# Kernel optimization log

Hardware: AMD Instinct MI355X
Metric: run time of the kernel (lower is better)

The kernel has to match this reference:

```python
import jax, jax.numpy as jnp
import numpy as np

N = 50000      # nodes
NE = 800000    # edges (avg degree 16)
DIN = 128      # in_dim / dim_edge
DOUT = 128     # out_dim (total)
H = 8          # heads
DH = DOUT // H # head dim = 16


def setup_inputs() -> dict:
    key = jax.random.key(0)
    ks = jax.random.split(key, 12)
    w = lambda k, shape: (jax.random.normal(k, shape, jnp.float32) / np.sqrt(shape[-1]))
    return {
        "x": jax.random.normal(ks[0], (N, DIN), jnp.float32),
        "edge_attr": jax.random.normal(ks[1], (NE, DIN), jnp.float32),
        "edge_index": jax.random.randint(ks[2], (2, NE), 0, N, dtype=jnp.int32),
        "batch_vec": jnp.zeros((N,), jnp.int32),  # single graph; only used for num_node
        "Wq": w(ks[3], (DOUT, DIN)), "bq": jnp.zeros((DOUT,), jnp.float32),
        "Wk": w(ks[4], (DOUT, DIN)), "bk": jnp.zeros((DOUT,), jnp.float32),
        "We": w(ks[5], (DOUT, DIN)), "be": jnp.zeros((DOUT,), jnp.float32),
        "Wv": w(ks[6], (DOUT, DIN)), "bv": jnp.zeros((DOUT,), jnp.float32),
    }


def reference(x, edge_attr, edge_index, batch_vec, Wq, bq, Wk, bk, We, be, Wv, bv):
    num_node = batch_vec.shape[0]
    # Node projections -> [N, H, DH]
    Qh = (x @ Wq.T + bq).reshape(-1, H, DH)
    Kh = (x @ Wk.T + bk).reshape(-1, H, DH)
    Vh = (x @ Wv.T + bv).reshape(-1, H, DH)
    # Edge projection -> [NE, H, DH]
    E = (edge_attr @ We.T + be).reshape(-1, H, DH)

    src = edge_index[0]
    dst = edge_index[1]
    # edge score: exp(clamp(sum(K_src * Q_dst / sqrt(DH) * E, -1), -5, 5))  [NE, H, 1]
    scale = 1.0 / np.sqrt(DH).astype(np.float32)
    s = jnp.sum((Kh[src] * Qh[dst]) * scale * E, axis=-1)
    score = jnp.exp(jnp.clip(s, -5.0, 5.0))[..., None]

    msg = Vh[src] * score                                   # [NE, H, DH]
    wV = jax.ops.segment_sum(msg, dst, num_segments=num_node)  # [N, H, DH]
    return wV.reshape(num_node, H * DH)
```

## Files before the change

### kernel.cpp

```cpp
#include <hip/hip_runtime.h>
#include <hip/hip_bf16.h>
#include <hip/hip_fp16.h>
#include <cstdint>


typedef float    f32x4  __attribute__((ext_vector_type(4)));
typedef short    bf16x8 __attribute__((ext_vector_type(8)));
typedef int      i32x4  __attribute__((ext_vector_type(4)));
typedef _Float16 f16x8  __attribute__((ext_vector_type(8)));
typedef _Float16 f16x4  __attribute__((ext_vector_type(4)));

#define AP 136
#define EP 132

__device__ __forceinline__ short f2bf(float f) {
    union { float f; uint32_t u; } v; v.f = f;
    uint32_t r = v.u + 0x7FFFu + ((v.u >> 16) & 1u);
    return (short)(r >> 16);
}
__device__ __forceinline__ float bf2f(short s) {
    union { uint32_t u; float f; } v; v.u = ((uint32_t)(uint16_t)s) << 16;
    return v.f;
}
__device__ __forceinline__ int cvt2(float a, float b) {
    float2 t; t.x = a; t.y = b;
    __hip_bfloat162 h = __float22bfloat162_rn(t);
    int r; __builtin_memcpy(&r, &h, 4);
    return r;
}
__device__ __forceinline__ float4 ntload4(const float* p) {
    i32x4 r = __builtin_nontemporal_load((const i32x4*)p);
    float4 f; __builtin_memcpy(&f, &r, 16);
    return f;
}

__global__ __launch_bounds__(256) void convert_weights(
        const float* __restrict__ Wq, const float* __restrict__ bq,
        const float* __restrict__ Wk, const float* __restrict__ bk,
        const float* __restrict__ We, const float* __restrict__ be,
        const float* __restrict__ Wv, const float* __restrict__ bv,
        const int* __restrict__ dstp, int NE,
        short* __restrict__ Whi, short* __restrict__ Wlo, float* __restrict__ ball,
        int* __restrict__ counts) {
    int idx = blockIdx.x * 256 + threadIdx.x;
    int wrow = idx >> 7;
    int k = idx & 127;
    int which = wrow >> 7;
    int r = wrow & 127;
    const float* Wsrc = which == 0 ? Wq : which == 1 ? Wk : which == 2 ? Wv : We;
    float f = Wsrc[r * 128 + k];
    short hi = f2bf(f);
    short lo = f2bf(f - bf2f(hi));
    Whi[idx] = hi; Wlo[idx] = lo;
    if (idx < 512) {
        int wh = idx >> 7; int rr = idx & 127;
        const float* bsrc = wh == 0 ? bq : wh == 1 ? bk : wh == 2 ? bv : be;
        ball[idx] = bsrc[rr];
    }
    for (int i = idx; i < NE; i += 65536)
        atomicAdd(&counts[dstp[i]], 1);
}

__global__ __launch_bounds__(1024) void scan1_kernel(const int* __restrict__ counts,
                                                     int* __restrict__ incl,
                                                     int* __restrict__ partials, int n) {
    __shared__ int sh[1024];
    int t = threadIdx.x;
    int i = blockIdx.x * 1024 + t;
    sh[t] = (i < n) ? counts[i] : 0;
    for (int off = 1; off < 1024; off <<= 1) {
        __syncthreads();
        int xv = (t >= off) ? sh[t - off] : 0;
        __syncthreads();
        sh[t] += xv;
    }
    __syncthreads();
    if (i < n) incl[i] = sh[t];
    if (t == 1023) partials[blockIdx.x] = sh[1023];
}

__global__ __launch_bounds__(1024) void scanB_kernel(const int* __restrict__ counts,
                                                     int* __restrict__ offsets,
                                                     int* __restrict__ cursors,
                                                     const int* __restrict__ partials,
                                                     int n, int total) {
    int pbase = 0;
    for (int b = 0; b < (int)blockIdx.x; ++b) pbase += partials[b];
    int i = blockIdx.x * 1024 + threadIdx.x;
    if (i < n) {
        int off = offsets[i] - counts[i] + pbase;
        offsets[i] = off;
        cursors[i] = off;
    } else if (i == n) {
        offsets[n] = total;
    }
}

__global__ __launch_bounds__(256, 4) void qkv_kernel(
        const float* __restrict__ x,
        const short* __restrict__ Whi, const short* __restrict__ Wlo,
        const float* __restrict__ ball,
        _Float16* __restrict__ Qb, _Float16* __restrict__ Kb, _Float16* __restrict__ Vb,
        int N) {
    __shared__ char lds[64 * AP * 2];
    const int t = threadIdx.x;
    const int m0 = blockIdx.x * 64;

#pragma unroll
    for (int i = 0; i < 4; ++i) {
        int g = t + i * 256;
        int row = g >> 4, c8 = g & 15;
        int grow = m0 + row;
        float4 f0 = {0.f,0.f,0.f,0.f}, f1 = {0.f,0.f,0.f,0.f};
        if (grow < N) {
            const float* p = x + (size_t)grow * 128 + c8 * 8;
            f0 = ntload4(p); f1 = ntload4(p + 4);
        }
        int4 v;
        v.x = cvt2(f0.x, f0.y); v.y = cvt2(f0.z, f0.w);
        v.z = cvt2(f1.x, f1.y); v.w = cvt2(f1.z, f1.w);
        *(int4*)(lds + row * (AP * 2) + c8 * 16) = v;
    }
    __syncthreads();

    const int w = t >> 6, lane = t & 63;
    const int r16 = lane & 15, g16 = lane >> 4;
    const int cb = w * 32;

    for (int ct = 0; ct < 3; ++ct) {
        const int colbase = ct * 128;
        f32x4 acc[4][2];
#pragma unroll
        for (int m = 0; m < 4; ++m)
#pragma unroll
            for (int n = 0; n < 2; ++n) acc[m][n] = (f32x4){0.f,0.f,0.f,0.f};

#pragma unroll
        for (int ks = 0; ks < 4; ++ks) {
            bf16x8 a[4];
#pragma unroll
            for (int m = 0; m < 4; ++m)
                a[m] = *(const bf16x8*)(lds + (m * 16 + r16) * (AP * 2) + ks * 64 + g16 * 16);
            bf16x8 bh2[2], bl2[2];
#pragma unroll
            for (int n = 0; n < 2; ++n) {
                int colg = colbase + cb + n * 16 + r16;
                bh2[n] = *(const bf16x8*)(Whi + colg * 128 + ks * 32 + g16 * 8);
                bl2[n] = *(const bf16x8*)(Wlo + colg * 128 + ks * 32 + g16 * 8);
            }
#pragma unroll
            for (int m = 0; m < 4; ++m)
#pragma unroll
                for (int n = 0; n < 2; ++n) {
                    acc[m][n] = __builtin_amdgcn_mfma_f32_16x16x32_bf16(a[m], bh2[n], acc[m][n], 0, 0, 0);
                    acc[m][n] = __builtin_amdgcn_mfma_f32_16x16x32_bf16(a[m], bl2[n], acc[m][n], 0, 0, 0);
                }
        }
        float bias[2];
#pragma unroll
        for (int n = 0; n < 2; ++n) bias[n] = ball[colbase + cb + n * 16 + r16];

        _Float16* outb = ct == 0 ? Qb : ct == 1 ? Kb : Vb;
#pragma unroll
        for (int m = 0; m < 4; ++m) {
            int grow = m0 + m * 16 + g16 * 4;
#pragma unroll
            for (int r = 0; r < 4; ++r) {
                if (grow + r < N) {
#pragma unroll
                    for (int n = 0; n < 2; ++n)
                        outb[(size_t)(grow + r) * 128 + cb + n * 16 + r16] =
                            (_Float16)(acc[m][n][r] + bias[n]);
                }
            }
        }
    }
}

__global__ __launch_bounds__(256) void edge_kernel(
        const float* __restrict__ ea,
        const int* __restrict__ srcp, const int* __restrict__ dstp,
        const short* __restrict__ Whi, const short* __restrict__ Wlo,
        const float* __restrict__ ball,
        const _Float16* __restrict__ Qb, const _Float16* __restrict__ Kb,
        float* __restrict__ scores, int* __restrict__ cursors,
        int2* __restrict__ ebuf, int NE) {
    __shared__ char lds[64 * EP * 4];
    const int t = threadIdx.x;
    const int e0 = blockIdx.x * 64;

    int sArr[2], dArr[2];
#pragma unroll
    for (int it = 0; it < 2; ++it) {
        int task = t + it * 256;
        int el = task >> 3, h = task & 7;
        int eg = e0 + el;
        bool ok = eg < NE;
        int s = ok ? srcp[eg] : 0;
        int d = ok ? dstp[eg] : 0;
        sArr[it] = s; dArr[it] = d;
        if (ok && h == 0) {
            int pos = atomicAdd(&cursors[d], 1);
            int2 v; v.x = s * 128; v.y = eg * 8;
            ebuf[pos] = v;
        }
    }

#pragma unroll
    for (int i = 0; i < 4; ++i) {
        int g = t + i * 256;
        int row = g >> 4, c8 = g & 15;
        int grow = e0 + row;
        float4 f0 = {0.f,0.f,0.f,0.f}, f1 = {0.f,0.f,0.f,0.f};
        if (grow < NE) {
            const float* p = ea + (size_t)grow * 128 + c8 * 8;
            f0 = ntload4(p); f1 = ntload4(p + 4);
        }
        int4 v;
        v.x = cvt2(f0.x, f0.y); v.y = cvt2(f0.z, f0.w);
        v.z = cvt2(f1.x, f1.y); v.w = cvt2(f1.z, f1.w);
        *(int4*)(lds + row * (AP * 2) + c8 * 16) = v;
    }
    __syncthreads();

    const int w = t >> 6, lane = t & 63;
    const int r16 = lane & 15, g16 = lane >> 4;
    const int cb = w * 32;

    f32x4 acc[4][2];
#pragma unroll
    for (int m = 0; m < 4; ++m)
#pragma unroll
        for (int n = 0; n < 2; ++n) acc[m][n] = (f32x4){0.f,0.f,0.f,0.f};

#pragma unroll
    for (int ks = 0; ks < 4; ++ks) {
        bf16x8 a[4];
#pragma unroll
        for (int m = 0; m < 4; ++m)
            a[m] = *(const bf16x8*)(lds + (m * 16 + r16) * (AP * 2) + ks * 64 + g16 * 16);
        bf16x8 bh2[2], bl2[2];
#pragma unroll
        for (int n = 0; n < 2; ++n) {
            int colg = 384 + cb + n * 16 + r16;
            bh2[n] = *(const bf16x8*)(Whi + colg * 128 + ks * 32 + g16 * 8);
            bl2[n] = *(const bf16x8*)(Wlo + colg * 128 + ks * 32 + g16 * 8);
        }
#pragma unroll
        for (int m = 0; m < 4; ++m)
#pragma unroll
            for (int n = 0; n < 2; ++n) {
                acc[m][n] = __builtin_amdgcn_mfma_f32_16x16x32_bf16(a[m], bh2[n], acc[m][n], 0, 0, 0);
                acc[m][n] = __builtin_amdgcn_mfma_f32_16x16x32_bf16(a[m], bl2[n], acc[m][n], 0, 0, 0);
            }
    }
    float bias[2];
#pragma unroll
    for (int n = 0; n < 2; ++n) bias[n] = ball[384 + cb + n * 16 + r16];

    __syncthreads();
    float* e_lds = (float*)lds;
#pragma unroll
    for (int m = 0; m < 4; ++m)
#pragma unroll
        for (int n = 0; n < 2; ++n)
#pragma unroll
            for (int r = 0; r < 4; ++r) {
                int row = m * 16 + g16 * 4 + r;
                int col = cb + n * 16 + r16;
                e_lds[row * EP + col] = acc[m][n][r] + bias[n];
            }
    __syncthreads();

#pragma unroll
    for (int it = 0; it < 2; ++it) {
        int task = t + it * 256;
        int el = task >> 3, h = task & 7;
        int eg = e0 + el;
        if (eg < NE) {
            const f16x8* Kp = (const f16x8*)(Kb + (size_t)sArr[it] * 128 + h * 16);
            const f16x8* Qp = (const f16x8*)(Qb + (size_t)dArr[it] * 128 + h * 16);
            f16x8 k0 = Kp[0], k1 = Kp[1];
            f16x8 q0 = Qp[0], q1 = Qp[1];
            float dot = 0.f;
#pragma unroll
            for (int j = 0; j < 2; ++j) {
                f32x4 ev0 = *(const f32x4*)(e_lds + el * EP + h * 16 + j * 8);
                f32x4 ev1 = *(const f32x4*)(e_lds + el * EP + h * 16 + j * 8 + 4);
                const f16x8& kk = j == 0 ? k0 : k1;
                const f16x8& qq = j == 0 ? q0 : q1;
#pragma unroll
                for (int r = 0; r < 4; ++r) {
                    dot += ev0[r] * (float)kk[r] * (float)qq[r];
                    dot += ev1[r] * (float)kk[r + 4] * (float)qq[r + 4];
                }
            }
            float sv = fminf(fmaxf(dot * 0.25f, -5.0f), 5.0f);
            scores[(size_t)eg * 8 + h] = __expf(sv);
        }
    }
}

__global__ __launch_bounds__(256) void gather_kernel(
        const int* __restrict__ offsets, const int2* __restrict__ eb,
        const float* __restrict__ scores, const _Float16* __restrict__ Vb,
        float* __restrict__ out, int N) {
    int node = blockIdx.x * 8 + (threadIdx.x >> 5);
    int c4 = threadIdx.x & 31;
    if (node >= N) return;
    int h = c4 >> 2;
    int beg = offsets[node], end = offsets[node + 1];
    f32x4 a0 = {0.f,0.f,0.f,0.f}, a1 = a0, a2 = a0, a3 = a0;
    int j = beg;
    auto vload = [&](int off) -> f32x4 {
        f16x4 v = *(const f16x4*)(Vb + off + c4 * 4);
        return (f32x4){(float)v[0], (float)v[1], (float)v[2], (float)v[3]};
    };
    for (; j + 8 <= end; j += 8) {
        int2 e0 = eb[j],     e1 = eb[j + 1], e2 = eb[j + 2], e3 = eb[j + 3];
        int2 e4 = eb[j + 4], e5 = eb[j + 5], e6 = eb[j + 6], e7 = eb[j + 7];
        f32x4 v0 = vload(e0.x), v1 = vload(e1.x), v2 = vload(e2.x), v3 = vload(e3.x);
        f32x4 v4 = vload(e4.x), v5 = vload(e5.x), v6 = vload(e6.x), v7 = vload(e7.x);
        a0 += scores[e0.y + h] * v0;
        a1 += scores[e1.y + h] * v1;
        a2 += scores[e2.y + h] * v2;
        a3 += scores[e3.y + h] * v3;
        a0 += scores[e4.y + h] * v4;
        a1 += scores[e5.y + h] * v5;
        a2 += scores[e6.y + h] * v6;
        a3 += scores[e7.y + h] * v7;
    }
    for (; j + 4 <= end; j += 4) {
        int2 e0 = eb[j], e1 = eb[j + 1], e2 = eb[j + 2], e3 = eb[j + 3];
        f32x4 v0 = vload(e0.x), v1 = vload(e1.x), v2 = vload(e2.x), v3 = vload(e3.x);
        a0 += scores[e0.y + h] * v0;
        a1 += scores[e1.y + h] * v1;
        a2 += scores[e2.y + h] * v2;
        a3 += scores[e3.y + h] * v3;
    }
    for (; j < end; ++j) {
        int2 e = eb[j];
        a0 += scores[e.y + h] * vload(e.x);
    }
    f32x4 sum = (a0 + a1) + (a2 + a3);
    *(f32x4*)(out + (size_t)node * 128 + c4 * 4) = sum;
}

extern "C" void kernel_launch(void* const* d_in, const int* in_sizes, int n_in,
                              void* d_out, int out_size, void* d_ws, size_t ws_size,
                              hipStream_t stream) {
    const float* x   = (const float*)d_in[0];
    const float* ea  = (const float*)d_in[1];
    const int* eidx  = (const int*)d_in[2];
    const float* Wq  = (const float*)d_in[4];  const float* bq = (const float*)d_in[5];
    const float* Wk  = (const float*)d_in[6];  const float* bk = (const float*)d_in[7];
    const float* We  = (const float*)d_in[8];  const float* be = (const float*)d_in[9];
    const float* Wv  = (const float*)d_in[10]; const float* bv = (const float*)d_in[11];
    const int N  = in_sizes[0] / 128;
    const int NE = in_sizes[2] / 2;
    const int* srcp = eidx;
    const int* dstp = eidx + NE;
    float* out = (float*)d_out;

    char* ws = (char*)d_ws;
    size_t o = 0;
    auto alloc = [&](size_t b) { size_t r = o; o += (b + 255) & ~(size_t)255; return r; };
    _Float16* Qb   = (_Float16*)(ws + alloc((size_t)N * 128 * 2));
    _Float16* Kb   = (_Float16*)(ws + alloc((size_t)N * 128 * 2));
    _Float16* Vb   = (_Float16*)(ws + alloc((size_t)N * 128 * 2));
    float* scores  = (float*)(ws + alloc((size_t)NE * 8 * 4));
    short* Whi     = (short*)(ws + alloc(512 * 128 * 2));
    short* Wlo     = (short*)(ws + alloc(512 * 128 * 2));
    float* ball    = (float*)(ws + alloc(512 * 4));
    int* counts    = (int*)(ws + alloc((size_t)(N + 1) * 4));
    int* offsets   = (int*)(ws + alloc((size_t)(N + 1) * 4));
    int* cursors   = (int*)(ws + alloc((size_t)N * 4));
    int2* ebuf     = (int2*)(ws + alloc((size_t)NE * 8));
    int* partials  = (int*)(ws + alloc(64 * 4));
    (void)ws_size; (void)n_in; (void)out_size;

    (void)hipMemsetAsync(counts, 0, (size_t)(N + 1) * 4, stream);

    convert_weights<<<256, 256, 0, stream>>>(Wq, bq, Wk, bk, We, be, Wv, bv,
                                             dstp, NE, Whi, Wlo, ball, counts);

    int nb = (N + 1023) / 1024;
    scan1_kernel<<<nb, 1024, 0, stream>>>(counts, offsets, partials, N);
    scanB_kernel<<<nb, 1024, 0, stream>>>(counts, offsets, cursors, partials, N, NE);

    qkv_kernel<<<(N + 63) / 64, 256, 0, stream>>>(x, Whi, Wlo, ball, Qb, Kb, Vb, N);

    edge_kernel<<<(NE + 63) / 64, 256, 0, stream>>>(ea, srcp, dstp, Whi, Wlo, ball,
                                                    Qb, Kb, scores, cursors, ebuf, NE);

    gather_kernel<<<(N + 7) / 8, 256, 0, stream>>>(offsets, ebuf, scores, Vb, out, N);
}
```

Measured before the change: 351.8 us.

## Process edges in destination-sorted order so scores are written contiguously per node

```diff
diff --git a/kernel.cpp b/kernel.cpp
--- a/kernel.cpp
+++ b/kernel.cpp
@@ -96,6 +96,22 @@
     }
 }
 
+__global__ __launch_bounds__(256) void scatter_kernel(
+        const int* __restrict__ srcp, const int* __restrict__ dstp,
+        int* __restrict__ cursors,
+        int* __restrict__ eord, int* __restrict__ esrc, int* __restrict__ edst,
+        int NE) {
+    int i = blockIdx.x * 256 + threadIdx.x;
+    if (i < NE) {
+        int d = dstp[i];
+        int s = srcp[i];
+        int pos = atomicAdd(&cursors[d], 1);
+        eord[pos] = i;
+        esrc[pos] = s * 128;
+        edst[pos] = d;
+    }
+}
+
 __global__ __launch_bounds__(256, 4) void qkv_kernel(
         const float* __restrict__ x,
         const short* __restrict__ Whi, const short* __restrict__ Wlo,
@@ -179,41 +195,25 @@
 
 __global__ __launch_bounds__(256) void edge_kernel(
         const float* __restrict__ ea,
-        const int* __restrict__ srcp, const int* __restrict__ dstp,
+        const int* __restrict__ eord, const int* __restrict__ esrc,
+        const int* __restrict__ edst,
         const short* __restrict__ Whi, const short* __restrict__ Wlo,
         const float* __restrict__ ball,
         const _Float16* __restrict__ Qb, const _Float16* __restrict__ Kb,
-        float* __restrict__ scores, int* __restrict__ cursors,
-        int2* __restrict__ ebuf, int NE) {
+        float* __restrict__ scores, int NE) {
     __shared__ char lds[64 * EP * 4];
     const int t = threadIdx.x;
     const int e0 = blockIdx.x * 64;
 
-    int sArr[2], dArr[2];
-#pragma unroll
-    for (int it = 0; it < 2; ++it) {
-        int task = t + it * 256;
-        int el = task >> 3, h = task & 7;
-        int eg = e0 + el;
-        bool ok = eg < NE;
-        int s = ok ? srcp[eg] : 0;
-        int d = ok ? dstp[eg] : 0;
-        sArr[it] = s; dArr[it] = d;
-        if (ok && h == 0) {
-            int pos = atomicAdd(&cursors[d], 1);
-            int2 v; v.x = s * 128; v.y = eg * 8;
-            ebuf[pos] = v;
-        }
-    }
-
 #pragma unroll
     for (int i = 0; i < 4; ++i) {
         int g = t + i * 256;
         int row = g >> 4, c8 = g & 15;
-        int grow = e0 + row;
+        int slot = e0 + row;
         float4 f0 = {0.f,0.f,0.f,0.f}, f1 = {0.f,0.f,0.f,0.f};
-        if (grow < NE) {
-            const float* p = ea + (size_t)grow * 128 + c8 * 8;
+        if (slot < NE) {
+            int eid = eord[slot];
+            const float* p = ea + (size_t)eid * 128 + c8 * 8;
             f0 = ntload4(p); f1 = ntload4(p + 4);
         }
         int4 v;
@@ -276,19 +276,21 @@
     for (int it = 0; it < 2; ++it) {
         int task = t + it * 256;
         int el = task >> 3, h = task & 7;
-        int eg = e0 + el;
-        if (eg < NE) {
-            const f16x8* Kp = (const f16x8*)(Kb + (size_t)sArr[it] * 128 + h * 16);
-            const f16x8* Qp = (const f16x8*)(Qb + (size_t)dArr[it] * 128 + h * 16);
+        int j = e0 + el;
+        if (j < NE) {
+            int s128 = esrc[j];
+            int d = edst[j];
+            const f16x8* Kp = (const f16x8*)(Kb + (size_t)s128 + h * 16);
+            const f16x8* Qp = (const f16x8*)(Qb + (size_t)d * 128 + h * 16);
             f16x8 k0 = Kp[0], k1 = Kp[1];
             f16x8 q0 = Qp[0], q1 = Qp[1];
             float dot = 0.f;
 #pragma unroll
-            for (int j = 0; j < 2; ++j) {
-                f32x4 ev0 = *(const f32x4*)(e_lds + el * EP + h * 16 + j * 8);
-                f32x4 ev1 = *(const f32x4*)(e_lds + el * EP + h * 16 + j * 8 + 4);
-                const f16x8& kk = j == 0 ? k0 : k1;
-                const f16x8& qq = j == 0 ? q0 : q1;
+            for (int jj = 0; jj < 2; ++jj) {
+                f32x4 ev0 = *(const f32x4*)(e_lds + el * EP + h * 16 + jj * 8);
+                f32x4 ev1 = *(const f32x4*)(e_lds + el * EP + h * 16 + jj * 8 + 4);
+                const f16x8& kk = jj == 0 ? k0 : k1;
+                const f16x8& qq = jj == 0 ? q0 : q1;
 #pragma unroll
                 for (int r = 0; r < 4; ++r) {
                     dot += ev0[r] * (float)kk[r] * (float)qq[r];
@@ -296,13 +298,13 @@
                 }
             }
             float sv = fminf(fmaxf(dot * 0.25f, -5.0f), 5.0f);
-            scores[(size_t)eg * 8 + h] = __expf(sv);
+            scores[(size_t)e0 * 8 + task] = __expf(sv);
         }
     }
 }
 
 __global__ __launch_bounds__(256) void gather_kernel(
-        const int* __restrict__ offsets, const int2* __restrict__ eb,
+        const int* __restrict__ offsets, const int* __restrict__ esrc,
         const float* __restrict__ scores, const _Float16* __restrict__ Vb,
         float* __restrict__ out, int N) {
     int node = blockIdx.x * 8 + (threadIdx.x >> 5);
@@ -317,30 +319,21 @@
         return (f32x4){(float)v[0], (float)v[1], (float)v[2], (float)v[3]};
     };
     for (; j + 8 <= end; j += 8) {
-        int2 e0 = eb[j],     e1 = eb[j + 1], e2 = eb[j + 2], e3 = eb[j + 3];
-        int2 e4 = eb[j + 4], e5 = eb[j + 5], e6 = eb[j + 6], e7 = eb[j + 7];
-        f32x4 v0 = vload(e0.x), v1 = vload(e1.x), v2 = vload(e2.x), v3 = vload(e3.x);
-        f32x4 v4 = vload(e4.x), v5 = vload(e5.x), v6 = vload(e6.x), v7 = vload(e7.x);
-        a0 += scores[e0.y + h] * v0;
-        a1 += scores[e1.y + h] * v1;
-        a2 += scores[e2.y + h] * v2;
-        a3 += scores[e3.y + h] * v3;
-        a0 += scores[e4.y + h] * v4;
-        a1 += scores[e5.y + h] * v5;
-        a2 += scores[e6.y + h] * v6;
-        a3 += scores[e7.y + h] * v7;
-    }
-    for (; j + 4 <= end; j += 4) {
-        int2 e0 = eb[j], e1 = eb[j + 1], e2 = eb[j + 2], e3 = eb[j + 3];
-        f32x4 v0 = vload(e0.x), v1 = vload(e1.x), v2 = vload(e2.x), v3 = vload(e3.x);
-        a0 += scores[e0.y + h] * v0;
-        a1 += scores[e1.y + h] * v1;
-        a2 += scores[e2.y + h] * v2;
-        a3 += scores[e3.y + h] * v3;
+        int s0 = esrc[j],     s1 = esrc[j + 1], s2 = esrc[j + 2], s3 = esrc[j + 3];
+        int s4 = esrc[j + 4], s5 = esrc[j + 5], s6 = esrc[j + 6], s7 = esrc[j + 7];
+        f32x4 v0 = vload(s0), v1 = vload(s1), v2 = vload(s2), v3 = vload(s3);
+        f32x4 v4 = vload(s4), v5 = vload(s5), v6 = vload(s6), v7 = vload(s7);
+        a0 += scores[(j    ) * 8 + h] * v0;
+        a1 += scores[(j + 1) * 8 + h] * v1;
+        a2 += scores[(j + 2) * 8 + h] * v2;
+        a3 += scores[(j + 3) * 8 + h] * v3;
+        a0 += scores[(j + 4) * 8 + h] * v4;
+        a1 += scores[(j + 5) * 8 + h] * v5;
+        a2 += scores[(j + 6) * 8 + h] * v6;
+        a3 += scores[(j + 7) * 8 + h] * v7;
     }
     for (; j < end; ++j) {
-        int2 e = eb[j];
-        a0 += scores[e.y + h] * vload(e.x);
+        a0 += scores[j * 8 + h] * vload(esrc[j]);
     }
     f32x4 sum = (a0 + a1) + (a2 + a3);
     *(f32x4*)(out + (size_t)node * 128 + c4 * 4) = sum;
@@ -375,7 +368,9 @@
     int* counts    = (int*)(ws + alloc((size_t)(N + 1) * 4));
     int* offsets   = (int*)(ws + alloc((size_t)(N + 1) * 4));
     int* cursors   = (int*)(ws + alloc((size_t)N * 4));
-    int2* ebuf     = (int2*)(ws + alloc((size_t)NE * 8));
+    int* eord      = (int*)(ws + alloc((size_t)NE * 4));
+    int* esrc      = (int*)(ws + alloc((size_t)NE * 4));
+    int* edst      = (int*)(ws + alloc((size_t)NE * 4));
     int* partials  = (int*)(ws + alloc(64 * 4));
     (void)ws_size; (void)n_in; (void)out_size;
 
@@ -388,10 +383,14 @@
     scan1_kernel<<<nb, 1024, 0, stream>>>(counts, offsets, partials, N);
     scanB_kernel<<<nb, 1024, 0, stream>>>(counts, offsets, cursors, partials, N, NE);
 
+    scatter_kernel<<<(NE + 255) / 256, 256, 0, stream>>>(srcp, dstp, cursors,
+                                                         eord, esrc, edst, NE);
+
     qkv_kernel<<<(N + 63) / 64, 256, 0, stream>>>(x, Whi, Wlo, ball, Qb, Kb, Vb, N);
 
-    edge_kernel<<<(NE + 63) / 64, 256, 0, stream>>>(ea, srcp, dstp, Whi, Wlo, ball,
-                                                    Qb, Kb, scores, cursors, ebuf, NE);
-
-    gather_kernel<<<(N + 7) / 8, 256, 0, stream>>>(offsets, ebuf, scores, Vb, out, N);
-}
+    edge_kernel<<<(NE + 63) / 64, 256, 0, stream>>>(ea, eord, esrc, edst,
+                                                    Whi, Wlo, ball, Qb, Kb,
+                                                    scores, NE);
+
+    gather_kernel<<<(N + 7) / 8, 256, 0, stream>>>(offsets, esrc, scores, Vb, out, N);
+}
```

After: 385.2 us. 1.09x slower.
